# Optimization experiments

Hardware: AMD Instinct MI355X
Metric: run time of the kernel (lower is better)

The kernel has to match this reference:

```python
import jax, jax.numpy as jnp
import numpy as np

B, D, UD = 32, 1024, 256          # batch, chunks_dim, units_dim
ENT, NENT = 32, 64                # entity_size, n_entities
S, C = NENT * ENT, NENT + 1       # src_len (units), n_chunks
NEG_INF = float('-inf')


def setup_inputs() -> dict:
    key = jax.random.key(0)
    ks = jax.random.split(key, 9)
    source = jax.random.normal(ks[0], (B, D), jnp.float32)
    high_level_repr = jax.random.normal(ks[1], (C, B, D), jnp.float32)
    pos_embs = jax.random.normal(ks[2], (S, B, UD), jnp.float32)
    low_level_repr = jax.random.normal(ks[3], (S, B, D), jnp.float32)
    low_level_mask = jax.random.randint(ks[4], (NENT, B, ENT), 0, 2).astype(bool)
    high_level_mask = jax.random.randint(ks[5], (1, B, C), 0, 2).astype(bool)
    high_level_mask = high_level_mask.at[..., 0].set(False)  # avoid all-masked chunk softmax
    W_unit = jax.random.normal(ks[6], (UD, D), jnp.float32) / np.sqrt(D)
    W_chunk = jax.random.normal(ks[7], (D, D), jnp.float32) / np.sqrt(D)
    W_out = jax.random.normal(ks[8], (D, 2 * D), jnp.float32) / np.sqrt(2 * D)
    return {"source": source, "high_level_repr": high_level_repr, "pos_embs": pos_embs,
            "low_level_repr": low_level_repr, "low_level_mask": low_level_mask,
            "high_level_mask": high_level_mask, "W_unit": W_unit, "W_chunk": W_chunk,
            "W_out": W_out}


def reference(source, high_level_repr, pos_embs, low_level_repr,
              low_level_mask, high_level_mask, W_unit, W_chunk, W_out):
    # batch-first views (torch transposes(0,1))
    hl = jnp.swapaxes(high_level_repr, 0, 1)    # (B, C, D)
    ll = jnp.swapaxes(low_level_repr, 0, 1)     # (B, S, D)
    pe = jnp.swapaxes(pos_embs, 0, 1)           # (B, S, UD)
    ll_mask = jnp.swapaxes(low_level_mask, 0, 1)   # (B, NENT, ENT)
    hl_mask = jnp.swapaxes(high_level_mask, 0, 1)  # (B, 1, C)

    # 'general' attention scorers, tgt_len == 1
    q_u = source @ W_unit.T                      # (B, UD)
    align_units = jnp.einsum('bd,bsd->bs', q_u, pe)        # (B, S)
    q_c = source @ W_chunk.T                     # (B, D)
    align_chunks = jnp.einsum('bd,bcd->bc', q_c, hl)[:, None, :]  # (B, 1, C)

    # low-level masked softmax per entity, NaN rows -> 0
    au = align_units.reshape(B, NENT, ENT)
    au = jnp.where(ll_mask, NEG_INF, au)
    au = jax.nn.softmax(au, axis=-1)
    all_masked = jnp.all(ll_mask, axis=-1)       # (B, NENT) rows that were NaN
    au = jnp.where(all_masked[..., None], 0.0, au)
    au = au.reshape(B, 1, S)

    # high-level masked softmax, drop chunk 0, inflate to unit granularity
    ac = jnp.where(hl_mask, NEG_INF, align_chunks)
    ac = jax.nn.softmax(ac, axis=-1)[:, :, 1:]   # (B, 1, C-1)
    ac_inflated = jnp.repeat(ac, ENT, axis=-1)   # (B, 1, S)

    align_vectors = ac_inflated * au             # (B, 1, S)
    c = jnp.einsum('bts,bsd->btd', align_vectors, ll)  # (B, 1, D)
    concat = jnp.concatenate([c, source[:, None, :]], axis=-1).reshape(B, 2 * D)
    attn_h = jnp.tanh(concat @ W_out.T)          # (B, D); tanh since attn_type='general'

    return (attn_h,
            align_vectors[:, 0, :],              # (B, S)
            ac[:, 0, :],                         # (B, C-1)
            au.reshape(B, S))                    # (B, S)
```

## Files before the change

### kernel.cpp

```cpp
#include <hip/hip_runtime.h>

#define B 32
#define D 1024
#define UD 256
#define ENT 32
#define NENT 64
#define S 2048
#define C 65

__device__ __forceinline__ float dot4(float4 w, const float* q) {
    return w.x * q[0] + w.y * q[1] + w.z * q[2] + w.w * q[3];
}

__global__ __launch_bounds__(256) void k_zero(float* __restrict__ p) {
    p[blockIdx.x * 256 + threadIdx.x] = 0.f;
}

__global__ __launch_bounds__(256) void k_proj(const float* __restrict__ src,
                                              const float* __restrict__ Wu,
                                              const float* __restrict__ Wc,
                                              float* __restrict__ qu,
                                              float* __restrict__ qc) {
    __shared__ alignas(16) float s_src[4][D];
    __shared__ float red[4][64][4];
    int t = threadIdx.x, rg = blockIdx.x, bg = blockIdx.y;
    for (int f = t; f < 4 * (D / 4); f += 256) {
        int bb = f >> 8, i4 = f & 255;
        float4 v = *(const float4*)(src + (size_t)(bg * 4 + bb) * D + i4 * 4);
        *(float4*)(&s_src[bb][i4 * 4]) = v;
    }
    __syncthreads();
    int jl = t & 63, kq = t >> 6;
    int gj = rg * 64 + jl;
    const float* wrow = (gj < UD) ? (Wu + (size_t)gj * D) : (Wc + (size_t)(gj - UD) * D);
    const float4* wp = (const float4*)wrow + kq * 64;
    float acc[4] = {0.f, 0.f, 0.f, 0.f};
#pragma unroll 4
    for (int i = 0; i < 64; ++i) {
        float4 w = wp[i];
        int k = kq * 256 + i * 4;
#pragma unroll
        for (int bb = 0; bb < 4; ++bb) acc[bb] += dot4(w, &s_src[bb][k]);
    }
#pragma unroll
    for (int bb = 0; bb < 4; ++bb) red[kq][jl][bb] = acc[bb];
    __syncthreads();
    {
        int jl2 = t & 63, bb = t >> 6;
        float s = red[0][jl2][bb] + red[1][jl2][bb] + red[2][jl2][bb] + red[3][jl2][bb];
        int gj2 = rg * 64 + jl2, b = bg * 4 + bb;
        if (gj2 < UD) qu[b * UD + gj2] = s;
        else qc[b * D + (gj2 - UD)] = s;
    }
}

__global__ __launch_bounds__(256) void k_units(const float* __restrict__ pe,
                                               const int* __restrict__ lmask,
                                               const float* __restrict__ qu,
                                               float* __restrict__ out_au) {
    __shared__ alignas(16) float q[UD];
    __shared__ float part[256];
    int n = blockIdx.x, b = blockIdx.y, t = threadIdx.x;
    q[t] = qu[b * UD + t];
    __syncthreads();
    int e = t >> 3, r = t & 7;
    const float4* pp = (const float4*)(pe + (size_t)(n * ENT + e) * B * UD + (size_t)b * UD) + r * 8;
    float acc = 0.f;
#pragma unroll
    for (int i = 0; i < 8; ++i) acc += dot4(pp[i], &q[(r * 8 + i) * 4]);
    part[t] = acc;
    __syncthreads();
    if (t < ENT) {
        float sc = 0.f;
#pragma unroll
        for (int r2 = 0; r2 < 8; ++r2) sc += part[t * 8 + r2];
        bool m = lmask[(size_t)n * B * ENT + b * ENT + t] != 0;
        float v = m ? -1e30f : sc;
        float mx = v;
        for (int o = 16; o >= 1; o >>= 1) mx = fmaxf(mx, __shfl_xor(mx, o));
        float p = m ? 0.f : __expf(v - mx);
        float sm = p;
        for (int o = 16; o >= 1; o >>= 1) sm += __shfl_xor(sm, o);
        out_au[b * S + n * ENT + t] = (sm > 0.f) ? (p / sm) : 0.f;
    }
}

__global__ __launch_bounds__(64) void k_cscore(const float* __restrict__ hl,
                                               const float* __restrict__ qc,
                                               float* __restrict__ scores) {
    int c = blockIdx.x, b = blockIdx.y, l = threadIdx.x;
    const float4* hp = (const float4*)(hl + (size_t)(c * B + b) * D);
    const float4* qp = (const float4*)(qc + (size_t)b * D);
    float acc = 0.f;
#pragma unroll
    for (int i = 0; i < 4; ++i) {
        int f = l + 64 * i;
        float4 h = hp[f], q = qp[f];
        acc += h.x * q.x + h.y * q.y + h.z * q.z + h.w * q.w;
    }
    for (int o = 32; o >= 1; o >>= 1) acc += __shfl_xor(acc, o);
    if (l == 0) scores[b * C + c] = acc;
}

__global__ __launch_bounds__(128) void k_csoft(const float* __restrict__ scores,
                                               const int* __restrict__ hmask,
                                               float* __restrict__ out_ac) {
    __shared__ float sc[C];
    __shared__ float red[2];
    int b = blockIdx.x, t = threadIdx.x;
    if (t < C) sc[t] = scores[b * C + t];
    __syncthreads();
    if (t == 0) {
        float mx = -1e30f;
        for (int c = 0; c < C; ++c) {
            float v = hmask[b * C + c] ? -1e30f : sc[c];
            mx = fmaxf(mx, v);
        }
        float sm = 0.f;
        for (int c = 0; c < C; ++c) {
            float v = hmask[b * C + c] ? -1e30f : sc[c];
            sm += __expf(v - mx);
        }
        red[0] = mx;
        red[1] = sm;
    }
    __syncthreads();
    if (t >= 1 && t < C) {
        bool m = hmask[b * C + t] != 0;
        float p = m ? 0.f : __expf(sc[t] - red[0]) / red[1];
        out_ac[b * NENT + (t - 1)] = p;
    }
}

__global__ __launch_bounds__(256) void k_ctx(const float* __restrict__ ll,
                                             const float* __restrict__ out_au,
                                             const float* __restrict__ out_ac,
                                             float* __restrict__ cf,
                                             float* __restrict__ out_av) {
    __shared__ float av[ENT];
    int n = blockIdx.x, b = blockIdx.y, t = threadIdx.x;
    if (t < ENT) {
        float a = out_ac[b * NENT + n] * out_au[b * S + n * ENT + t];
        av[t] = a;
        out_av[b * S + n * ENT + t] = a;
    }
    __syncthreads();
    float a0 = 0.f, a1 = 0.f, a2 = 0.f, a3 = 0.f;
    const float* base = ll + (size_t)(n * ENT) * B * D + (size_t)b * D + t * 4;
#pragma unroll 4
    for (int e = 0; e < ENT; ++e) {
        float4 x = *(const float4*)(base + (size_t)e * B * D);
        float wv = av[e];
        a0 += wv * x.x;
        a1 += wv * x.y;
        a2 += wv * x.z;
        a3 += wv * x.w;
    }
    float* cp = cf + b * D + t * 4;
    atomicAdd(cp + 0, a0);
    atomicAdd(cp + 1, a1);
    atomicAdd(cp + 2, a2);
    atomicAdd(cp + 3, a3);
}

__global__ __launch_bounds__(256) void k_out(const float* __restrict__ Wo,
                                             const float* __restrict__ src,
                                             const float* __restrict__ cf,
                                             float* __restrict__ out_h) {
    __shared__ alignas(16) float cc[4][2 * D];
    __shared__ float red[4][64][4];
    int t = threadIdx.x, jg = blockIdx.x, bg = blockIdx.y;
    for (int f = t; f < 4 * (2 * D / 4); f += 256) {
        int bb = f >> 9, part = f & 511;
        int b = bg * 4 + bb;
        float4 v;
        if (part < 256) v = *(const float4*)(cf + (size_t)b * D + part * 4);
        else v = *(const float4*)(src + (size_t)b * D + (part - 256) * 4);
        *(float4*)(&cc[bb][part * 4]) = v;
    }
    __syncthreads();
    int jl = t & 63, kq = t >> 6;
    int j = jg * 64 + jl;
    const float4* wp = (const float4*)(Wo + (size_t)j * 2 * D) + kq * 128;
    float acc[4] = {0.f, 0.f, 0.f, 0.f};
#pragma unroll 4
    for (int i = 0; i < 128; ++i) {
        float4 w = wp[i];
        int k = kq * 512 + i * 4;
#pragma unroll
        for (int bb = 0; bb < 4; ++bb) acc[bb] += dot4(w, &cc[bb][k]);
    }
#pragma unroll
    for (int bb = 0; bb < 4; ++bb) red[kq][jl][bb] = acc[bb];
    __syncthreads();
    {
        int jl2 = t & 63, bb = t >> 6;
        float s = red[0][jl2][bb] + red[1][jl2][bb] + red[2][jl2][bb] + red[3][jl2][bb];
        out_h[(size_t)(bg * 4 + bb) * D + jg * 64 + jl2] = tanhf(s);
    }
}

extern "C" void kernel_launch(void* const* d_in, const int* in_sizes, int n_in,
                              void* d_out, int out_size, void* d_ws, size_t ws_size,
                              hipStream_t stream) {
    const float* src = (const float*)d_in[0];
    const float* hl = (const float*)d_in[1];
    const float* pe = (const float*)d_in[2];
    const float* ll = (const float*)d_in[3];
    const int* lmask = (const int*)d_in[4];
    const int* hmask = (const int*)d_in[5];
    const float* Wu = (const float*)d_in[6];
    const float* Wc = (const float*)d_in[7];
    const float* Wo = (const float*)d_in[8];

    float* out = (float*)d_out;
    float* out_h = out;
    float* out_av = out + B * D;
    float* out_ac = out_av + B * S;
    float* out_au = out_ac + B * NENT;

    float* ws = (float*)d_ws;
    float* qu = ws;
    float* qc = qu + B * UD;
    float* cf = qc + B * D;
    float* scores = cf + B * D;

    k_zero<<<dim3(B * D / 256), 256, 0, stream>>>(cf);
    k_proj<<<dim3(20, 8), 256, 0, stream>>>(src, Wu, Wc, qu, qc);
    k_units<<<dim3(NENT, B), 256, 0, stream>>>(pe, lmask, qu, out_au);
    k_cscore<<<dim3(C, B), 64, 0, stream>>>(hl, qc, scores);
    k_csoft<<<dim3(B), 128, 0, stream>>>(scores, hmask, out_ac);
    k_ctx<<<dim3(NENT, B), 256, 0, stream>>>(ll, out_au, out_ac, cf, out_av);
    k_out<<<dim3(16, 8), 256, 0, stream>>>(Wo, src, cf, out_h);
}
```

Baseline: 479.9 us.

## Fuse chunk score and softmax; replace atomic context reduction with two-stage partial sums

Merges the chunk-score and chunk-softmax kernels into a single per-batch kernel that stages the query in shared memory. The context kernel now processes 256 units per block, writes partial sums to a workspace, and a new reduction kernel sums the 8 partials, which removes the zero-init kernel and the atomics. The context kernel drops from 2048 blocks to 256 blocks that each stream 256 rows, so far less parallelism is available to hide memory latency on a bandwidth-bound 256MB read. The chunk kernel is also limited to 32 blocks.

```diff
diff --git a/kernel.cpp b/kernel.cpp
--- a/kernel.cpp
+++ b/kernel.cpp
@@ -10,10 +10,6 @@
 
 __device__ __forceinline__ float dot4(float4 w, const float* q) {
     return w.x * q[0] + w.y * q[1] + w.z * q[2] + w.w * q[3];
-}
-
-__global__ __launch_bounds__(256) void k_zero(float* __restrict__ p) {
-    p[blockIdx.x * 256 + threadIdx.x] = 0.f;
 }
 
 __global__ __launch_bounds__(256) void k_proj(const float* __restrict__ src,
@@ -85,30 +81,30 @@
     }
 }
 
-__global__ __launch_bounds__(64) void k_cscore(const float* __restrict__ hl,
-                                               const float* __restrict__ qc,
-                                               float* __restrict__ scores) {
-    int c = blockIdx.x, b = blockIdx.y, l = threadIdx.x;
-    const float4* hp = (const float4*)(hl + (size_t)(c * B + b) * D);
-    const float4* qp = (const float4*)(qc + (size_t)b * D);
-    float acc = 0.f;
-#pragma unroll
-    for (int i = 0; i < 4; ++i) {
-        int f = l + 64 * i;
-        float4 h = hp[f], q = qp[f];
-        acc += h.x * q.x + h.y * q.y + h.z * q.z + h.w * q.w;
-    }
-    for (int o = 32; o >= 1; o >>= 1) acc += __shfl_xor(acc, o);
-    if (l == 0) scores[b * C + c] = acc;
-}
-
-__global__ __launch_bounds__(128) void k_csoft(const float* __restrict__ scores,
-                                               const int* __restrict__ hmask,
-                                               float* __restrict__ out_ac) {
+__global__ __launch_bounds__(256) void k_chunks(const float* __restrict__ hl,
+                                                const int* __restrict__ hmask,
+                                                const float* __restrict__ qc,
+                                                float* __restrict__ out_ac) {
+    __shared__ alignas(16) float q[D];
     __shared__ float sc[C];
     __shared__ float red[2];
     int b = blockIdx.x, t = threadIdx.x;
-    if (t < C) sc[t] = scores[b * C + t];
+    for (int i = t; i < D / 4; i += 256)
+        *(float4*)(&q[i * 4]) = *(const float4*)(qc + (size_t)b * D + i * 4);
+    __syncthreads();
+    int w = t >> 6, l = t & 63;
+    for (int c = w; c < C; c += 4) {
+        const float4* hp = (const float4*)(hl + (size_t)(c * B + b) * D);
+        float acc = 0.f;
+#pragma unroll
+        for (int i = 0; i < 4; ++i) {
+            int f = l + 64 * i;
+            float4 h = hp[f];
+            acc += dot4(h, &q[f * 4]);
+        }
+        for (int o = 32; o >= 1; o >>= 1) acc += __shfl_xor(acc, o);
+        if (l == 0) sc[c] = acc;
+    }
     __syncthreads();
     if (t == 0) {
         float mx = -1e30f;
@@ -135,32 +131,39 @@
 __global__ __launch_bounds__(256) void k_ctx(const float* __restrict__ ll,
                                              const float* __restrict__ out_au,
                                              const float* __restrict__ out_ac,
-                                             float* __restrict__ cf,
+                                             float* __restrict__ pf,
                                              float* __restrict__ out_av) {
-    __shared__ float av[ENT];
-    int n = blockIdx.x, b = blockIdx.y, t = threadIdx.x;
-    if (t < ENT) {
-        float a = out_ac[b * NENT + n] * out_au[b * S + n * ENT + t];
-        av[t] = a;
-        out_av[b * S + n * ENT + t] = a;
-    }
-    __syncthreads();
-    float a0 = 0.f, a1 = 0.f, a2 = 0.f, a3 = 0.f;
-    const float* base = ll + (size_t)(n * ENT) * B * D + (size_t)b * D + t * 4;
-#pragma unroll 4
-    for (int e = 0; e < ENT; ++e) {
-        float4 x = *(const float4*)(base + (size_t)e * B * D);
-        float wv = av[e];
-        a0 += wv * x.x;
-        a1 += wv * x.y;
-        a2 += wv * x.z;
-        a3 += wv * x.w;
-    }
-    float* cp = cf + b * D + t * 4;
-    atomicAdd(cp + 0, a0);
-    atomicAdd(cp + 1, a1);
-    atomicAdd(cp + 2, a2);
-    atomicAdd(cp + 3, a3);
+    __shared__ float s_av[256];
+    int ss = blockIdx.x, b = blockIdx.y, t = threadIdx.x;
+    {
+        int s = ss * 256 + t;
+        int n = s >> 5;
+        float a = out_ac[b * NENT + n] * out_au[b * S + s];
+        s_av[t] = a;
+        out_av[b * S + s] = a;
+    }
+    __syncthreads();
+    float4 acc = {0.f, 0.f, 0.f, 0.f};
+    const float4* base = (const float4*)(ll + (size_t)(ss * 256) * B * D + (size_t)b * D) + t;
+#pragma unroll 8
+    for (int j = 0; j < 256; ++j) {
+        float4 x = base[(size_t)j * (B * D / 4)];
+        float wv = s_av[j];
+        acc.x += wv * x.x;
+        acc.y += wv * x.y;
+        acc.z += wv * x.z;
+        acc.w += wv * x.w;
+    }
+    *(float4*)(pf + (size_t)ss * B * D + (size_t)b * D + t * 4) = acc;
+}
+
+__global__ __launch_bounds__(256) void k_red(const float* __restrict__ pf,
+                                             float* __restrict__ cf) {
+    int f = blockIdx.x * 256 + threadIdx.x;
+    float s = 0.f;
+#pragma unroll
+    for (int ss = 0; ss < 8; ++ss) s += pf[(size_t)ss * B * D + f];
+    cf[f] = s;
 }
 
 __global__ __launch_bounds__(256) void k_out(const float* __restrict__ Wo,
@@ -223,13 +226,12 @@
     float* qu = ws;
     float* qc = qu + B * UD;
     float* cf = qc + B * D;
-    float* scores = cf + B * D;
-
-    k_zero<<<dim3(B * D / 256), 256, 0, stream>>>(cf);
+    float* pf = cf + B * D;
+
     k_proj<<<dim3(20, 8), 256, 0, stream>>>(src, Wu, Wc, qu, qc);
     k_units<<<dim3(NENT, B), 256, 0, stream>>>(pe, lmask, qu, out_au);
-    k_cscore<<<dim3(C, B), 64, 0, stream>>>(hl, qc, scores);
-    k_csoft<<<dim3(B), 128, 0, stream>>>(scores, hmask, out_ac);
-    k_ctx<<<dim3(NENT, B), 256, 0, stream>>>(ll, out_au, out_ac, cf, out_av);
+    k_chunks<<<dim3(B), 256, 0, stream>>>(hl, hmask, qc, out_ac);
+    k_ctx<<<dim3(8, B), 256, 0, stream>>>(ll, out_au, out_ac, pf, out_av);
+    k_red<<<dim3(B * D / 256), 256, 0, stream>>>(pf, cf);
     k_out<<<dim3(16, 8), 256, 0, stream>>>(Wo, src, cf, out_h);
 }
```

Result: no change. 478.0 us (-0.4%).
